# Performance work log

Hardware: AMD Instinct MI355X
Metric: run time of the kernel (lower is better)

The kernel has to match this reference:

```python
import jax, jax.numpy as jnp
import numpy as np

B, C, V, K, H, W = 1, 3, 9, 8, 512, 512


def setup_inputs() -> dict:
    key = jax.random.key(0)
    k0, k1 = jax.random.split(key, 2)
    x = jax.random.normal(k0, (B, C, K, H, W), jnp.float32)          # FDL layers (spatial)
    y_views = jax.random.normal(k1, (B, C, V, H, W), jnp.float32)    # observed views (spatial)
    g = jnp.arange(3, dtype=jnp.float32) - 1.0                       # 3x3 camera grid positions
    uu, vv = jnp.meshgrid(g, g, indexing='ij')
    u = uu.reshape(-1)
    v = vv.reshape(-1)
    d = jnp.linspace(-2.0, 2.0, K).astype(jnp.float32)               # d_fdl disparities
    rho = jnp.full((1,), 0.3, jnp.float32)
    return {"x": x, "y_views": y_views, "u": u, "v": v, "d": d, "rho": rho}


def _pack_half_spectrum(Xf, x_c, y_c, n_proc):
    # [..., H, W] -> transpose to [..., W, H], center-roll so zero freq is at (x_c-1, y_c-1),
    # flatten x-major, keep the non-redundant half spectrum (first n_proc entries).
    Xt = jnp.swapaxes(Xf, -1, -2)
    Xt = jnp.roll(Xt, shift=(x_c - 1, y_c - 1), axis=(-2, -1))
    sh = Xt.shape
    return Xt.reshape(sh[:-2] + (sh[-2] * sh[-1],))[..., :n_proc]


def reference(x, y_views, u, v, d, rho):
    Bn, Cn, Kn = x.shape[0], x.shape[1], x.shape[2]
    Hn, Wn = x.shape[-2], x.shape[-1]
    rho = rho.reshape(())
    x_c = (Wn + 2) // 2                      # ceil((W+1)/2)
    y_c = (Hn + 2) // 2
    n_proc = Hn * (x_c - 1) + y_c            # half-spectrum size
    e0 = 1 - Hn % 2
    e1 = 1 - Wn % 2

    X = jnp.fft.fft2(x)                      # [B,C,K,H,W] complex64
    Y = jnp.fft.fft2(y_views)                # [B,C,V,H,W] complex64
    Xp = jnp.moveaxis(_pack_half_spectrum(X, x_c, y_c, n_proc), 2, 3) * rho   # [B,C,F,K]
    Yp = jnp.moveaxis(_pack_half_spectrum(Y, x_c, y_c, n_proc), 2, 3)         # [B,C,F,V]

    # centered angular frequency grids, flattened x-major to match packing order
    wx = (jnp.arange(Wn, dtype=jnp.float32) - (x_c - 1)) * (2.0 * np.pi / Wn)
    wy = (jnp.arange(Hn, dtype=jnp.float32) - (y_c - 1)) * (2.0 * np.pi / Hn)
    wx_f = jnp.repeat(wx, Hn)[:n_proc]       # [F]
    wy_f = jnp.tile(wy, Wn)[:n_proc]         # [F]

    # FDL data matrix A[f,v,k] = exp(i * d_k * (u_v*wx_f + v_v*wy_f))
    shift = u[None, :] * wx_f[:, None] + v[None, :] * wy_f[:, None]   # [F,V]
    A = jnp.exp(1j * shift[:, :, None] * d[None, None, :])            # [F,V,K] complex64
    Ah = jnp.conj(A)
    ATA = jnp.einsum('fvk,fvl->fkl', Ah, A)                           # [F,K,K]
    ATb = jnp.einsum('fvk,bcfv->bcfk', Ah, Yp)                        # [B,C,F,K]
    M = ATA + rho * jnp.eye(Kn, dtype=ATA.dtype)
    fdl = jnp.linalg.solve(M, (ATb + Xp)[..., None])[..., 0]          # [B,C,F,K]

    # pad redundant half with zeros, restore [B,C,K,H,W] layout
    fdl = jnp.pad(fdl, ((0, 0), (0, 0), (0, Hn * Wn - n_proc), (0, 0)))
    fdl = fdl.reshape(Bn, Cn, Wn, Hn, Kn).transpose(0, 1, 4, 3, 2)    # [B,C,K,H,W]

    # Hermitian (conjugate) symmetry reconstruction
    fdl = fdl.at[..., y_c:, x_c - 1:].set(jnp.conj(fdl[..., e0:y_c - 1, e1:x_c][..., ::-1, ::-1]))
    fdl = fdl.at[..., e0:y_c, x_c:].set(jnp.conj(fdl[..., y_c - 1:, e1:x_c - 1][..., ::-1, ::-1]))
    fdl = jnp.roll(fdl, shift=(1 - y_c, 1 - x_c), axis=(-2, -1))
    return jnp.fft.ifft2(fdl).real
```

## Files before the change

kernel.cpp:

```cpp
#include <hip/hip_runtime.h>
#include <math.h>

constexpr int N    = 512;
constexpr int LOGN = 9;
constexpr int NN   = N * N;
constexpr int CCH  = 3;
constexpr int KK   = 8;
constexpr int VV   = 9;
constexpr int FHALF = N * (N / 2) + (N / 2 + 1);
constexpr int NS   = 257;
constexpr int RW   = 544;
constexpr float PI_F = 3.14159265358979323846f;

__device__ __forceinline__ float2 cmulf(float2 a, float2 b) {
    return make_float2(a.x * b.x - a.y * b.y, a.x * b.y + a.y * b.x);
}
__device__ __forceinline__ float2 cadd(float2 a, float2 b) { return make_float2(a.x + b.x, a.y + b.y); }
__device__ __forceinline__ float2 csub(float2 a, float2 b) { return make_float2(a.x - b.x, a.y - b.y); }

template<int SG>
__device__ __forceinline__ float2 cmuli(float2 z) {
    return (SG < 0) ? make_float2(z.y, -z.x) : make_float2(-z.y, z.x);
}

template<int SG>
__device__ __forceinline__ void dft8(float2 x[8]) {
    const float c = 0.70710678118654752440f;
    float2 a0 = cadd(x[0], x[4]), a1 = cadd(x[1], x[5]);
    float2 a2 = cadd(x[2], x[6]), a3 = cadd(x[3], x[7]);
    float2 d0 = csub(x[0], x[4]), d1 = csub(x[1], x[5]);
    float2 d2 = csub(x[2], x[6]), d3 = csub(x[3], x[7]);
    float2 b0 = d0;
    float2 b1 = cmulf(d1, make_float2(c, (float)SG * c));
    float2 b2 = cmuli<SG>(d2);
    float2 b3 = cmulf(d3, make_float2(-c, (float)SG * c));
    float2 aa0 = cadd(a0, a2), aa1 = cadd(a1, a3);
    float2 ab0 = csub(a0, a2), ab1 = cmuli<SG>(csub(a1, a3));
    float2 ba0 = cadd(b0, b2), ba1 = cadd(b1, b3);
    float2 bb0 = csub(b0, b2), bb1 = cmuli<SG>(csub(b1, b3));
    x[0] = cadd(aa0, aa1); x[4] = csub(aa0, aa1);
    x[2] = cadd(ab0, ab1); x[6] = csub(ab0, ab1);
    x[1] = cadd(ba0, ba1); x[5] = csub(ba0, ba1);
    x[3] = cadd(bb0, bb1); x[7] = csub(bb0, bb1);
}

__device__ __forceinline__ void twiddle8(float2 v[8], float base) {
    float sn, cs;
    __sincosf(base, &sn, &cs);
    float2 w1 = make_float2(cs, sn);
    float2 wk = w1;
    v[1] = cmulf(v[1], wk);
    #pragma unroll
    for (int k = 2; k < 8; ++k) { wk = cmulf(wk, w1); v[k] = cmulf(v[k], wk); }
}

template<int SG>
__device__ __forceinline__ void wave_fft512(float2 v[8], float* sre, float* sim,
                                            int t, int stride, int off) {
    int t1 = t >> 3, t0 = t & 7;
    dft8<SG>(v);
    twiddle8(v, (float)SG * (2.0f * PI_F / 512.0f) * (float)t);
    #pragma unroll
    for (int k = 0; k < 8; ++k) {
        int a = (68 * k + 8 * t1 + t0) * stride + off;
        sre[a] = v[k].x; sim[a] = v[k].y;
    }
    #pragma unroll
    for (int n = 0; n < 8; ++n) {
        int a = (68 * t1 + 8 * n + t0) * stride + off;
        v[n] = make_float2(sre[a], sim[a]);
    }
    dft8<SG>(v);
    twiddle8(v, (float)SG * (2.0f * PI_F / 64.0f) * (float)t0);
    #pragma unroll
    for (int k = 0; k < 8; ++k) {
        int a = (68 * t0 + 8 * k + t1) * stride + off;
        sre[a] = v[k].x; sim[a] = v[k].y;
    }
    #pragma unroll
    for (int n = 0; n < 8; ++n) {
        int a = (68 * n + 8 * t0 + t1) * stride + off;
        v[n] = make_float2(sre[a], sim[a]);
    }
    dft8<SG>(v);
}

__global__ __launch_bounds__(256) void k_fft_r2c_rows_pack_T(const float* __restrict__ inx,
                                                             const float* __restrict__ iny,
                                                             int nximg,
                                                             float2* __restrict__ outT) {
    __shared__ float ure[2313];
    __shared__ float uim[2313];
    int w = threadIdx.x >> 6, t = threadIdx.x & 63;
    int blk = blockIdx.x;
    int img = blk >> 6;
    int rowbase = (blk & 63) << 3;
    long long row0 = (long long)blk * 8 + 2 * w;
    long long xrows = (long long)nximg * N;
    const float* src0 = (row0 < xrows) ? (inx + row0 * N)
                                       : (iny + (row0 - xrows) * N);
    const float* src1 = src0 + N;
    float* sre = ure + w * 544;
    float* sim = uim + w * 544;
    float2 v[8];
    #pragma unroll
    for (int e = 0; e < 8; ++e) v[e] = make_float2(src0[t + 64 * e], src1[t + 64 * e]);
    wave_fft512<-1>(v, sre, sim, t, 1, 0);
    int kb = (t >> 3) + 8 * (t & 7);
    #pragma unroll
    for (int k0 = 0; k0 < 8; ++k0) {
        int p = kb + 64 * k0;
        sre[p] = v[k0].x; sim[p] = v[k0].y;
    }
    float2 r0v[4], r1v[4];
    #pragma unroll
    for (int k0 = 4; k0 < 8; ++k0) {
        int p  = kb + 64 * k0;
        int mp = 512 - p;
        float zmx = sre[mp], zmy = sim[mp];
        float2 Zp = v[k0];
        r0v[k0 - 4] = make_float2(0.5f * (Zp.x + zmx), 0.5f * (Zp.y - zmy));
        r1v[k0 - 4] = make_float2(0.5f * (Zp.y + zmy), 0.5f * (zmx - Zp.x));
    }
    float2 z0 = v[0];
    __syncthreads();
    #pragma unroll
    for (int k0 = 0; k0 < 4; ++k0) {
        int s = kb + 64 * k0;
        ure[s * 9 + 2 * w]     = r0v[k0].x; uim[s * 9 + 2 * w]     = r0v[k0].y;
        ure[s * 9 + 2 * w + 1] = r1v[k0].x; uim[s * 9 + 2 * w + 1] = r1v[k0].y;
    }
    if (t == 0) {
        ure[256 * 9 + 2 * w]     = z0.x; uim[256 * 9 + 2 * w]     = 0.0f;
        ure[256 * 9 + 2 * w + 1] = z0.y; uim[256 * 9 + 2 * w + 1] = 0.0f;
    }
    __syncthreads();
    float2* dst = outT + (long long)img * ((long long)NS * N);
    int tt = threadIdx.x;
    int r2 = (tt & 3) << 1;
    #pragma unroll
    for (int j = 0; j < 4; ++j) {
        int s = j * 64 + (tt >> 2);
        *(float4*)&dst[s * N + rowbase + r2] =
            make_float4(ure[s * 9 + r2],     uim[s * 9 + r2],
                        ure[s * 9 + r2 + 1], uim[s * 9 + r2 + 1]);
    }
    if (tt < 4) {
        int r2b = tt << 1;
        *(float4*)&dst[256 * N + rowbase + r2b] =
            make_float4(ure[256 * 9 + r2b],     uim[256 * 9 + r2b],
                        ure[256 * 9 + r2b + 1], uim[256 * 9 + r2b + 1]);
    }
}

__global__ __launch_bounds__(256) void k_fft_r2c_rows(const float* __restrict__ in,
                                                      float2* __restrict__ out) {
    __shared__ float sre[4][544];
    __shared__ float sim[4][544];
    int w = threadIdx.x >> 6, t = threadIdx.x & 63;
    long long grow = (long long)blockIdx.x * 4 + w;
    const float* src = in + grow * N;
    float2 v[8];
    #pragma unroll
    for (int e = 0; e < 8; ++e) v[e] = make_float2(src[t + 64 * e], 0.0f);
    wave_fft512<-1>(v, sre[w], sim[w], t, 1, 0);
    float2* dst = out + grow * N;
    int kb = (t >> 3) + 8 * (t & 7);
    #pragma unroll
    for (int k0 = 0; k0 < 8; ++k0) dst[kb + 64 * k0] = v[k0];
}

template<int SG>
__global__ __launch_bounds__(256) void k_fft_pairswap(float2* __restrict__ data,
                                                      float scale, int lex, int sex) {
    __shared__ float sre[4][544];
    __shared__ float sim[4][544];
    int w = threadIdx.x >> 6, t = threadIdx.x & 63;
    int b = blockIdx.x;
    long long imgBase = (long long)(b >> 7) * NN;
    int pa = (b & 127) << 1;
    int rowg = pa + (w & 1) + ((w >> 1) << 8);
    const float2* src = data + imgBase + (long long)rowg * N;
    float2 v[8];
    #pragma unroll
    for (int e = 0; e < 8; ++e) v[e] = src[t + 64 * (e ^ lex)];
    __syncthreads();
    wave_fft512<SG>(v, sre[w], sim[w], t, 1, 0);
    float2* dst = data + imgBase + (long long)(rowg ^ 256) * N;
    int kb = (t >> 3) + 8 * (t & 7);
    #pragma unroll
    for (int k0 = 0; k0 < 8; ++k0) {
        float2 z = v[k0];
        dst[kb + 64 * (k0 ^ sex)] = make_float2(z.x * scale, z.y * scale);
    }
}

__device__ __forceinline__ void accum_pair(float2 bacc[KK], float tr[KK], float s,
                                           float d0, float dlt, float2 Yp, float2 Yn) {
    float2 Sp = make_float2(Yp.x + Yn.x, Yp.y + Yn.y);
    float2 Dm = make_float2(Yp.x - Yn.x, Yp.y - Yn.y);
    float sn, cs;
    __sincosf(s * d0, &sn, &cs);  float2 p = make_float2(cs, sn);
    __sincosf(s * dlt, &sn, &cs); float2 q = make_float2(cs, sn);
    float2 w = q;
    #pragma unroll
    for (int k = 0; k < KK; ++k) {
        bacc[k].x += p.x * Sp.x + p.y * Dm.y;
        bacc[k].y += p.x * Sp.y - p.y * Dm.x;
        if (k < KK - 1) {
            p = cmulf(p, q);
            tr[k + 1] += 2.0f * w.x;
            w = cmulf(w, q);
        }
    }
}

__device__ __forceinline__ void solve_point(float2 bacc[KK], float tr[KK], float rho) {
    float diag = tr[0] + rho;
    float L[36], Li[KK];
    #pragma unroll
    for (int j = 0; j < KK; ++j) {
        float acc = diag;
        #pragma unroll
        for (int t = 0; t < j; ++t) { float l = L[(j * (j - 1)) / 2 + t]; acc -= l * l; }
        float dj = sqrtf(acc);
        float inv = 1.0f / dj;
        Li[j] = inv;
        #pragma unroll
        for (int i = j + 1; i < KK; ++i) {
            float a = tr[i - j];
            #pragma unroll
            for (int t = 0; t < j; ++t)
                a -= L[(i * (i - 1)) / 2 + t] * L[(j * (j - 1)) / 2 + t];
            L[(i * (i - 1)) / 2 + j] = a * inv;
        }
    }
    #pragma unroll
    for (int i = 0; i < KK; ++i) {
        float2 a = bacc[i];
        #pragma unroll
        for (int t = 0; t < i; ++t) {
            float l = L[(i * (i - 1)) / 2 + t];
            a.x -= l * bacc[t].x;
            a.y -= l * bacc[t].y;
        }
        bacc[i] = make_float2(a.x * Li[i], a.y * Li[i]);
    }
    #pragma unroll
    for (int i = KK - 1; i >= 0; --i) {
        float2 a = bacc[i];
        #pragma unroll
        for (int t = i + 1; t < KK; ++t) {
            float l = L[(t * (t - 1)) / 2 + i];
            a.x -= l * bacc[t].x;
            a.y -= l * bacc[t].y;
        }
        bacc[i] = make_float2(a.x * Li[i], a.y * Li[i]);
    }
}

__global__ __launch_bounds__(512, 4) void k_fused_solve(const float2* __restrict__ Rt,
                                                        float2* __restrict__ P,
                                                        float2* __restrict__ S0,
                                                        int nximg,
                                                        const float* __restrict__ uu,
                                                        const float* __restrict__ vvp,
                                                        const float* __restrict__ dd,
                                                        const float* __restrict__ rhop) {
    __shared__ float bre[VV][RW];
    __shared__ float bim[VV][RW];
    int a  = blockIdx.x;
    int ch = blockIdx.y;
    int t  = threadIdx.x;
    int w = t >> 6, lane = t & 63;
    int kb = (lane >> 3) + 8 * (lane & 7);
    const long long LN = (long long)NS * N;

    float2 fvX[8];
    {
        const float2* srcX = Rt + (long long)(ch * KK + w) * LN + (long long)a * N;
        #pragma unroll
        for (int e = 0; e < 8; ++e) fvX[e] = srcX[lane + 64 * e];
    }

    {
        int ybase = nximg + ch * VV;
        #pragma unroll
        for (int rep = 0; rep < 2; ++rep) {
            int vimg = w + 8 * rep;
            if (vimg < VV) {
                const float2* src = Rt + (long long)(ybase + vimg) * LN + (long long)a * N;
                float2 fv[8];
                #pragma unroll
                for (int e = 0; e < 8; ++e) fv[e] = src[lane + 64 * e];
                wave_fft512<-1>(fv, bre[vimg], bim[vimg], lane, 1, 0);
                #pragma unroll
                for (int k0 = 0; k0 < 8; ++k0) {
                    int pos = kb + 64 * (k0 ^ 4);
                    bre[vimg][pos] = fv[k0].x; bim[vimg][pos] = fv[k0].y;
                }
            }
        }
    }
    __syncthreads();

    float rho = rhop[0];
    float d0 = dd[0], dlt = dd[1] - dd[0];
    const float C = 2.0f * PI_F / (float)N;
    float wxv = (float)(a - 256) * C;
    float wy  = (float)(t - 256) * C;
    float2 bacc[KK];
    float tr[KK];
    {
        float2 yc = make_float2(bre[4][t], bim[4][t]);
        #pragma unroll
        for (int k = 0; k < KK; ++k) bacc[k] = yc;
        tr[0] = (float)VV;
        #pragma unroll
        for (int l = 1; l < KK; ++l) tr[l] = 1.0f;
    }
    #pragma unroll
    for (int j = 0; j < 4; ++j) {
        int vp = 5 + j, vn = 3 - j;
        accum_pair(bacc, tr, uu[vp] * wxv + vvp[vp] * wy, d0, dlt,
                   make_float2(bre[vp][t], bim[vp][t]),
                   make_float2(bre[vn][t], bim[vn][t]));
    }
    __syncthreads();

    {
        wave_fft512<-1>(fvX, bre[w], bim[w], lane, 1, 0);
        #pragma unroll
        for (int k0 = 0; k0 < 8; ++k0) {
            int pos = kb + 64 * (k0 ^ 4);
            bre[w][pos] = fvX[k0].x; bim[w][pos] = fvX[k0].y;
        }
    }
    __syncthreads();

    #pragma unroll
    for (int k = 0; k < KK; ++k) {
        bacc[k].x += rho * bre[k][t];
        bacc[k].y += rho * bim[k][t];
    }
    solve_point(bacc, tr, rho);
    #pragma unroll
    for (int k = 0; k < KK; ++k) {
        bre[k][t] = bacc[k].x;
        bim[k][t] = bacc[k].y;
    }
    __syncthreads();

    {
        const float inv512 = 1.0f / 512.0f;
        int k = w;
        bool selfm = (a == 256);
        float2 v[8];
        #pragma unroll
        for (int e = 0; e < 8; ++e) {
            int idx = (lane + 64 * e) ^ 256;
            if (selfm && idx >= 257) {
                int bs = 512 - idx;
                v[e] = make_float2(bre[k][bs], -bim[k][bs]);
            } else {
                v[e] = make_float2(bre[k][idx], bim[k][idx]);
            }
        }
        float s0x = bre[k][0], s0y = bim[k][0];
        wave_fft512<1>(v, bre[k], bim[k], lane, 1, 0);
        if (lane == 0)
            S0[(long long)(ch * KK + k) * 257 + a] =
                make_float2(s0x * inv512, s0y * inv512);
        float2* Pimg = P + (long long)(ch * KK + k) * NN;
        int prow = (a >= 1 && a <= 255) ? (a + 256) : (a == 0 ? 256 : 0);
        float2* pmain = Pimg + (long long)prow * N;
        #pragma unroll
        for (int k0 = 0; k0 < 8; ++k0) {
            int pos = kb + 64 * k0;
            float2 W = v[k0];
            pmain[pos] = make_float2(W.x * inv512, W.y * inv512);
        }
    }
}

__global__ __launch_bounds__(256) void k_fft_cols_inv_real(const float2* __restrict__ in,
                                                           const float2* __restrict__ T0,
                                                           float* __restrict__ out,
                                                           float scale) {
    __shared__ float tre[4896];
    __shared__ float tim[4896];
    int t = threadIdx.x;
    long long imgOff = (long long)blockIdx.y * NN;
    int b0 = blockIdx.x << 3;
    {
        int xi2 = (t & 3) << 1;
        int yb  = t >> 2;
        const float2* img = in + imgOff;
        const float2* T0i = T0 + (long long)blockIdx.y * 257;
        #pragma unroll
        for (int it = 0; it < 4; ++it) {
            int p = 256 + it * 64 + yb;
            float4 q = *(const float4*)&img[(long long)p * N + b0 + xi2];
            int c = p * 9 + xi2;
            tre[c] = q.x; tim[c] = q.y; tre[c + 1] = q.z; tim[c + 1] = q.w;
            if (p > 256) {
                float2 t0 = T0i[p - 256];
                int m0 = b0 + xi2;
                float sg0 = (m0 & 1) ? -1.0f : 1.0f;
                float sg1 = -sg0;
                int cm = (512 - p) * 9 + xi2;
                tre[cm]     = q.x - t0.x * sg0;
                tim[cm]     = -q.y + t0.y * sg0;
                tre[cm + 1] = q.z - t0.x * sg1;
                tim[cm + 1] = -q.w + t0.y * sg1;
            }
        }
        if (t < 4) {
            int xi2b = t << 1;
            float4 q = *(const float4*)&img[(long long)(b0 + xi2b)];
            tre[xi2b] = q.x; tim[xi2b] = q.y; tre[xi2b + 1] = q.z; tim[xi2b + 1] = q.w;
        }
    }
    __syncthreads();
    int w = t >> 6, lane = t & 63;
    int kb = (lane >> 3) + 8 * (lane & 7);
    #pragma unroll
    for (int r = 0; r < 2; ++r) {
        int cc = (w << 1) | r;
        float2 v[8];
        #pragma unroll
        for (int e = 0; e < 8; ++e) {
            int a = (lane + 64 * e) * 9 + cc;
            v[e] = make_float2(tre[a], tim[a]);
        }
        wave_fft512<1>(v, tre, tim, lane, 9, cc);
        #pragma unroll
        for (int k0 = 0; k0 < 8; ++k0)
            tre[(kb + 64 * k0) * 9 + cc] = v[k0].x;
    }
    __syncthreads();
    {
        int xi = t >> 5, co = t & 31;
        float* orow = out + (long long)blockIdx.y * NN + (long long)(b0 + xi) * N;
        #pragma unroll
        for (int it = 0; it < 4; ++it) {
            int ww = it * 128 + co * 4;
            *(float4*)&orow[ww] = make_float4(tre[ww * 9 + xi] * scale,
                                              tre[(ww + 1) * 9 + xi] * scale,
                                              tre[(ww + 2) * 9 + xi] * scale,
                                              tre[(ww + 3) * 9 + xi] * scale);
        }
    }
}

__global__ __launch_bounds__(256) void k_transpose_inplace(float2* __restrict__ data) {
    int ti = blockIdx.x, tj = blockIdx.y;
    if (ti > tj) return;
    float2* img = data + (long long)blockIdx.z * NN;
    __shared__ float2 ta[32][33];
    __shared__ float2 tb[32][33];
    int tx = threadIdx.x, ty = threadIdx.y;
    int r0 = ti << 5, c0 = tj << 5;
    bool diag = (ti == tj);
    #pragma unroll
    for (int kk = 0; kk < 4; ++kk) {
        int r = ty + (kk << 3);
        ta[r][tx] = img[(long long)(r0 + r) * N + (c0 + tx)];
        if (!diag) tb[r][tx] = img[(long long)(c0 + r) * N + (r0 + tx)];
    }
    __syncthreads();
    #pragma unroll
    for (int kk = 0; kk < 4; ++kk) {
        int r = ty + (kk << 3);
        img[(long long)(c0 + r) * N + (r0 + tx)] = ta[tx][r];
        if (!diag) img[(long long)(r0 + r) * N + (c0 + tx)] = tb[tx][r];
    }
}

__global__ __launch_bounds__(256) void k_fft_c2r_rows(const float2* __restrict__ in,
                                                      float* __restrict__ out, float scale) {
    __shared__ float sre[4][544];
    __shared__ float sim[4][544];
    int w = threadIdx.x >> 6, t = threadIdx.x & 63;
    long long grow = (long long)blockIdx.x * 4 + w;
    const float2* src = in + grow * N;
    float2 v[8];
    #pragma unroll
    for (int e = 0; e < 8; ++e) v[e] = src[t + 64 * e];
    wave_fft512<1>(v, sre[w], sim[w], t, 1, 0);
    float* dst = out + grow * N;
    int kb = (t >> 3) + 8 * (t & 7);
    #pragma unroll
    for (int k0 = 0; k0 < 8; ++k0) dst[kb + 64 * k0] = v[k0].x * scale;
}

__global__ __launch_bounds__(256) void k_solve(float2* __restrict__ Xs,
                                               const float2* __restrict__ Ys,
                                               const float* __restrict__ uu,
                                               const float* __restrict__ vv,
                                               const float* __restrict__ dd,
                                               const float* __restrict__ rhop) {
    int f = blockIdx.x * 256 + threadIdx.x;
    if (f >= FHALF) return;
    long long coffX = (long long)blockIdx.y * KK * NN;
    long long coffY = (long long)blockIdx.y * VV * NN;
    float rho = rhop[0];
    int x = f >> LOGN;
    int y = f & (N - 1);
    float wxv = (float)(x - N / 2) * (2.0f * PI_F / (float)N);
    float wyv = (float)(y - N / 2) * (2.0f * PI_F / (float)N);
    float d0 = dd[0], dlt = dd[1] - dd[0];
    float2 bacc[KK];
    float tr[KK];
    {
        float2 Yc = Ys[coffY + (long long)4 * NN + f];
        #pragma unroll
        for (int k = 0; k < KK; ++k) bacc[k] = Yc;
        tr[0] = (float)VV;
        #pragma unroll
        for (int l = 1; l < KK; ++l) tr[l] = 1.0f;
    }
    #pragma unroll
    for (int j = 0; j < 4; ++j) {
        int vp = 5 + j, vn = 3 - j;
        float s = uu[vp] * wxv + vv[vp] * wyv;
        accum_pair(bacc, tr, s, d0, dlt,
                   Ys[coffY + (long long)vp * NN + f],
                   Ys[coffY + (long long)vn * NN + f]);
    }
    #pragma unroll
    for (int k = 0; k < KK; ++k) {
        float2 Xk = Xs[coffX + (long long)k * NN + f];
        bacc[k].x += rho * Xk.x;
        bacc[k].y += rho * Xk.y;
    }
    solve_point(bacc, tr, rho);
    int xm = (N - x) & (N - 1);
    int ym = (N - y) & (N - 1);
    long long fm = (long long)xm * N + ym;
    bool conjMirror = false, zeroMirror = false;
    if (x >= 1 && x <= N / 2 - 1) {
        if (y == 0) zeroMirror = true; else conjMirror = true;
    } else if (x == N / 2 && y >= 1 && y <= N / 2 - 1) {
        conjMirror = true;
    }
    #pragma unroll
    for (int k = 0; k < KK; ++k) {
        float2* base = Xs + coffX + (long long)k * NN;
        float2 z = bacc[k];
        base[f] = z;
        if (conjMirror)      base[fm] = make_float2(z.x, -z.y);
        else if (zeroMirror) base[fm] = make_float2(0.f, 0.f);
    }
}

extern "C" void kernel_launch(void* const* d_in, const int* in_sizes, int n_in,
                              void* d_out, int out_size, void* d_ws, size_t ws_size,
                              hipStream_t stream) {
    (void)in_sizes; (void)n_in; (void)out_size;
    const float* x   = (const float*)d_in[0];
    const float* yv  = (const float*)d_in[1];
    const float* uu  = (const float*)d_in[2];
    const float* vvp = (const float*)d_in[3];
    const float* dd  = (const float*)d_in[4];
    const float* rho = (const float*)d_in[5];
    float* out = (float*)d_out;
    float2* ws = (float2*)d_ws;

    const float invN = 1.0f / (float)N;
    const size_t lnPer = (size_t)NS * N;
    const size_t needBatched =
        ((size_t)CCH * (KK + VV) * lnPer + (size_t)CCH * KK * NN
         + (size_t)CCH * KK * 257) * sizeof(float2);
    const size_t needChan =
        ((size_t)(KK + VV) * lnPer + (size_t)KK * NN
         + (size_t)KK * 257) * sizeof(float2);

    if (ws_size >= needChan) {
        bool batched = ws_size >= needBatched;
        int iters = batched ? 1 : CCH;
        int ncs   = batched ? CCH : 1;
        int nx = ncs * KK, ny = ncs * VV;
        for (int it = 0; it < iters; ++it) {
            float2* Rt = ws;
            float2* P  = ws + (size_t)(nx + ny) * lnPer;
            float2* S0 = P  + (size_t)nx * NN;
            const float* xin = x  + (size_t)it * KK * NN;
            const float* yin = yv + (size_t)it * VV * NN;
            float* oout = out + (size_t)it * KK * NN;
            k_fft_r2c_rows_pack_T<<<(nx + ny) * 64, 256, 0, stream>>>(xin, yin, nx, Rt);
            k_fused_solve<<<dim3(257, ncs), 512, 0, stream>>>(Rt, P, S0, nx,
                                                              uu, vvp, dd, rho);
            k_fft_cols_inv_real<<<dim3(N / 8, nx), 256, 0, stream>>>(P, S0, oout, invN);
        }
    } else {
        for (int it = 0; it < CCH; ++it) {
            float2* Xb = ws;
            float2* Yb = ws + (size_t)KK * NN;
            const float* xin = x  + (size_t)it * KK * NN;
            const float* yin = yv + (size_t)it * VV * NN;
            float* oout = out + (size_t)it * KK * NN;
            k_fft_r2c_rows<<<KK * (N / 4), 256, 0, stream>>>(xin, Xb);
            k_fft_r2c_rows<<<VV * (N / 4), 256, 0, stream>>>(yin, Yb);
            k_transpose_inplace<<<dim3(16, 16, KK), dim3(32, 8), 0, stream>>>(Xb);
            k_transpose_inplace<<<dim3(16, 16, VV), dim3(32, 8), 0, stream>>>(Yb);
            k_fft_pairswap<-1><<<KK * (N / 4), 256, 0, stream>>>(Xb, 1.0f, 0, 4);
            k_fft_pairswap<-1><<<VV * (N / 4), 256, 0, stream>>>(Yb, 1.0f, 0, 4);
            k_solve<<<dim3((FHALF + 255) / 256, 1), 256, 0, stream>>>(Xb, Yb, uu, vvp, dd, rho);
            k_fft_pairswap<1><<<KK * (N / 4), 256, 0, stream>>>(Xb, invN, 4, 0);
            k_transpose_inplace<<<dim3(16, 16, KK), dim3(32, 8), 0, stream>>>(Xb);
            k_fft_c2r_rows<<<KK * (N / 4), 256, 0, stream>>>(Xb, oout, invN);
        }
    }
}
```

Before: 157.0 us.

## Pack two real-output columns per complex inverse FFT in column pass

The inverse column FFT kernel now combines two adjacent columns into one complex sequence (first as real part, second as imaginary part) before the 512-point FFT. Each block covers 16 output rows instead of 8 using the same 8 FFTs, and the real and imaginary parts of each result are written out as two separate real rows. The aim is to halve the FFT arithmetic and shared-memory work per output, since the output is real. In exchange it adds extra arithmetic to form the packed Hermitian inputs, and the grid has half as many blocks.

Result: faster. 153.6 us (-2.2%).

```diff
diff --git a/kernel.cpp b/kernel.cpp
--- a/kernel.cpp
+++ b/kernel.cpp
@@ -391,34 +391,31 @@
     __shared__ float tim[4896];
     int t = threadIdx.x;
     long long imgOff = (long long)blockIdx.y * NN;
-    int b0 = blockIdx.x << 3;
-    {
-        int xi2 = (t & 3) << 1;
-        int yb  = t >> 2;
+    int b0 = blockIdx.x << 4;
+    {
+        int xi = t & 7;
+        int yb = t >> 3;
         const float2* img = in + imgOff;
         const float2* T0i = T0 + (long long)blockIdx.y * 257;
         #pragma unroll
-        for (int it = 0; it < 4; ++it) {
-            int p = 256 + it * 64 + yb;
-            float4 q = *(const float4*)&img[(long long)p * N + b0 + xi2];
-            int c = p * 9 + xi2;
-            tre[c] = q.x; tim[c] = q.y; tre[c + 1] = q.z; tim[c + 1] = q.w;
-            if (p > 256) {
+        for (int it = 0; it < 8; ++it) {
+            int p = 256 + it * 32 + yb;
+            float4 q = *(const float4*)&img[(long long)p * N + b0 + 2 * xi];
+            int c = p * 9 + xi;
+            if (p == 256) {
+                tre[c] = q.x; tim[c] = q.z;
+            } else {
                 float2 t0 = T0i[p - 256];
-                int m0 = b0 + xi2;
-                float sg0 = (m0 & 1) ? -1.0f : 1.0f;
-                float sg1 = -sg0;
-                int cm = (512 - p) * 9 + xi2;
-                tre[cm]     = q.x - t0.x * sg0;
-                tim[cm]     = -q.y + t0.y * sg0;
-                tre[cm + 1] = q.z - t0.x * sg1;
-                tim[cm + 1] = -q.w + t0.y * sg1;
+                float h1x = q.x - 0.5f * t0.x, h1y = q.y - 0.5f * t0.y;
+                float h2x = q.z + 0.5f * t0.x, h2y = q.w + 0.5f * t0.y;
+                tre[c] = h1x - h2y; tim[c] = h1y + h2x;
+                int cm = (512 - p) * 9 + xi;
+                tre[cm] = h1x + h2y; tim[cm] = h2x - h1y;
             }
         }
-        if (t < 4) {
-            int xi2b = t << 1;
-            float4 q = *(const float4*)&img[(long long)(b0 + xi2b)];
-            tre[xi2b] = q.x; tim[xi2b] = q.y; tre[xi2b + 1] = q.z; tim[xi2b + 1] = q.w;
+        if (t < 8) {
+            float4 q = *(const float4*)&img[b0 + 2 * t];
+            tre[t] = q.x; tim[t] = q.z;
         }
     }
     __syncthreads();
@@ -435,20 +432,26 @@
         }
         wave_fft512<1>(v, tre, tim, lane, 9, cc);
         #pragma unroll
-        for (int k0 = 0; k0 < 8; ++k0)
-            tre[(kb + 64 * k0) * 9 + cc] = v[k0].x;
-    }
-    __syncthreads();
-    {
-        int xi = t >> 5, co = t & 31;
-        float* orow = out + (long long)blockIdx.y * NN + (long long)(b0 + xi) * N;
-        #pragma unroll
-        for (int it = 0; it < 4; ++it) {
-            int ww = it * 128 + co * 4;
-            *(float4*)&orow[ww] = make_float4(tre[ww * 9 + xi] * scale,
-                                              tre[(ww + 1) * 9 + xi] * scale,
-                                              tre[(ww + 2) * 9 + xi] * scale,
-                                              tre[(ww + 3) * 9 + xi] * scale);
+        for (int k0 = 0; k0 < 8; ++k0) {
+            int pos = (kb + 64 * k0) * 9 + cc;
+            tre[pos] = v[k0].x;
+            tim[pos] = v[k0].y;
+        }
+    }
+    __syncthreads();
+    {
+        int rr = t >> 4;
+        int co = t & 15;
+        int slot = rr >> 1;
+        const float* src = (rr & 1) ? tim : tre;
+        float* orow = out + (long long)blockIdx.y * NN + (long long)(b0 + rr) * N;
+        #pragma unroll
+        for (int itw = 0; itw < 8; ++itw) {
+            int n = itw * 64 + co * 4;
+            *(float4*)&orow[n] = make_float4(src[n * 9 + slot] * scale,
+                                             src[(n + 1) * 9 + slot] * scale,
+                                             src[(n + 2) * 9 + slot] * scale,
+                                             src[(n + 3) * 9 + slot] * scale);
         }
     }
 }
@@ -591,7 +594,7 @@
             k_fft_r2c_rows_pack_T<<<(nx + ny) * 64, 256, 0, stream>>>(xin, yin, nx, Rt);
             k_fused_solve<<<dim3(257, ncs), 512, 0, stream>>>(Rt, P, S0, nx,
                                                               uu, vvp, dd, rho);
-            k_fft_cols_inv_real<<<dim3(N / 8, nx), 256, 0, stream>>>(P, S0, oout, invN);
+            k_fft_cols_inv_real<<<dim3(N / 16, nx), 256, 0, stream>>>(P, S0, oout, invN);
         }
     } else {
         for (int it = 0; it < CCH; ++it) {
```
